# Kernel tuning notes

Hardware: AMD Instinct MI355X
Metric: run time of the kernel (lower is better)

## Reference

```python
import jax, jax.numpy as jnp
import numpy as np

D, K, B, IMG, NCH = 128, 512, 8, 128, 3


def adder2d(x, w, k, stride, pad):
    # AdderNet L1 'convolution': y[b,co,l] = -sum_p |patch[b,p,l] - w[co,p]|
    # x: [B,C,H,W], w: [Cout, C*k*k]
    p = jax.lax.conv_general_dilated_patches(x, (k, k), (stride, stride), [(pad, pad), (pad, pad)])
    Bb, P, Ho, Wo = p.shape
    p = p.reshape(Bb, P, Ho * Wo)  # [B, C*k*k, L]
    def one(wc):  # wc: [P] -> [B, L]; sequential over Cout to bound memory
        return -jnp.sum(jnp.abs(p - wc[None, :, None]), axis=1)
    o = jax.lax.map(one, w)  # [Cout, B, L]
    return jnp.transpose(o, (1, 0, 2)).reshape(Bb, w.shape[0], Ho, Wo)


def bn(x, g, b, eps=1e-5):
    # eval-mode BatchNorm2d with running_mean=0, running_var=1
    s = g * jax.lax.rsqrt(jnp.asarray(1.0 + eps, x.dtype))
    return x * s[None, :, None, None] + b[None, :, None, None]


def conv2d(x, w, b, pad):
    y = jax.lax.conv_general_dilated(x, w, (1, 1), [(pad, pad), (pad, pad)],
                                     dimension_numbers=('NCHW', 'OIHW', 'NCHW'))
    return y + b[None, :, None, None]


def up2x(x):  # nn.Upsample(scale_factor=2, bilinear, align_corners=False)
    Bb, C, H, W = x.shape
    return jax.image.resize(x, (Bb, C, 2 * H, 2 * W), method='bilinear')


def adder_resblock(x, w1, w2, g, b):
    # [ReLU, adder3x3, BN, ReLU, adder1x1] + residual
    h = jax.nn.relu(x)
    h = adder2d(h, w1, 3, 1, 1)
    h = bn(h, g, b)
    h = jax.nn.relu(h)
    h = adder2d(h, w2, 1, 1, 0)
    return x + h


def conv_resblock(x, w1, b1, w2, b2):
    # [ReLU, conv3x3, ReLU, conv1x1] + residual (bn=False in decoder)
    h = jax.nn.relu(x)
    h = conv2d(h, w1, b1, 1)
    h = jax.nn.relu(h)
    h = conv2d(h, w2, b2, 0)
    return x + h


def vq_forward(z_e, E):
    # NearestEmbed: E is [d, k]
    Bb, C, H, W = z_e.shape
    flat = jnp.transpose(z_e, (0, 2, 3, 1)).reshape(-1, C)  # [N, d]
    d2 = (jnp.sum(flat * flat, axis=1, keepdims=True)
          - 2.0 * (flat @ E) + jnp.sum(E * E, axis=0)[None, :])  # [N, k]
    argmin = jnp.argmin(d2, axis=1)  # [N]
    q = jnp.take(E.T, argmin, axis=0)  # [N, d]
    # weight_sg=True path: straight-through to z_e, no grad to E
    zq_flat = flat + jax.lax.stop_gradient(q - flat)
    z_q = jnp.transpose(zq_flat.reshape(Bb, H, W, C), (0, 3, 1, 2))
    # emb path: z_e detached, grad flows to E through the gather
    emb = jnp.transpose(q.reshape(Bb, H, W, C), (0, 3, 1, 2))
    return z_q, emb, argmin.reshape(Bb, H, W)


def reference(x, we1, we2, ae1_w1, ae1_w2, ae2_w1, ae2_w2, bn_gamma, bn_beta,
              emb_weight, rd1_w1, rd1_b1, rd1_w2, rd1_b2, rd2_w1, rd2_b1,
              rd2_w2, rd2_b2, cd1_w, cd1_b, cd2_w, cd2_b):
    g, b = bn_gamma, bn_beta
    h = adder2d(x, we1, 4, 2, 1)
    h = jax.nn.relu(bn(h, g[0], b[0]))
    h = adder2d(h, we2, 4, 2, 1)
    h = jax.nn.relu(bn(h, g[1], b[1]))
    h = adder_resblock(h, ae1_w1, ae1_w2, g[2], b[2])
    h = bn(h, g[3], b[3])
    h = adder_resblock(h, ae2_w1, ae2_w2, g[4], b[4])
    z_e = bn(h, g[5], b[5])  # bne4 (gamma = 1/40)

    z_q, emb, argmin = vq_forward(z_e, emb_weight)

    y = conv_resblock(z_q, rd1_w1, rd1_b1, rd1_w2, rd1_b2)
    y = bn(y, g[6], b[6])
    y = conv_resblock(y, rd2_w1, rd2_b1, rd2_w2, rd2_b2)
    y = up2x(y)
    y = conv2d(y, cd1_w, cd1_b, 1)
    y = jax.nn.relu(bn(y, g[7], b[7]))
    y = up2x(y)
    y = conv2d(y, cd2_w, cd2_b, 1)
    y = jnp.tanh(y)
    return (y, z_e, emb, argmin)


def setup_inputs() -> dict:
    key = jax.random.key(0)
    ks = jax.random.split(key, 16)
    f = lambda k, shp: (0.02 * jax.random.normal(k, shp)).astype(jnp.float32)
    inp = {}
    inp['x'] = jax.random.normal(ks[0], (B, NCH, IMG, IMG), jnp.float32)
    inp['we1'] = f(ks[1], (D, NCH * 16))       # adder 4x4 s2
    inp['we2'] = f(ks[2], (D, D * 16))
    inp['ae1_w1'] = f(ks[3], (D, D * 9))       # adder 3x3
    inp['ae1_w2'] = f(ks[4], (D, D))           # adder 1x1
    inp['ae2_w1'] = f(ks[5], (D, D * 9))
    inp['ae2_w2'] = f(ks[6], (D, D))
    inp['bn_gamma'] = jnp.ones((8, D), jnp.float32).at[5].set(1.0 / 40.0)
    inp['bn_beta'] = jnp.zeros((8, D), jnp.float32)
    inp['emb_weight'] = f(ks[7], (D, K))
    inp['rd1_w1'] = f(ks[8], (D, D, 3, 3)); inp['rd1_b1'] = jnp.zeros(D, jnp.float32)
    inp['rd1_w2'] = f(ks[9], (D, D, 1, 1)); inp['rd1_b2'] = jnp.zeros(D, jnp.float32)
    inp['rd2_w1'] = f(ks[10], (D, D, 3, 3)); inp['rd2_b1'] = jnp.zeros(D, jnp.float32)
    inp['rd2_w2'] = f(ks[11], (D, D, 1, 1)); inp['rd2_b2'] = jnp.zeros(D, jnp.float32)
    inp['cd1_w'] = f(ks[12], (D, D, 3, 3)); inp['cd1_b'] = jnp.zeros(D, jnp.float32)
    inp['cd2_w'] = f(ks[13], (NCH, D, 3, 3)); inp['cd2_b'] = jnp.zeros(NCH, jnp.float32)
    return inp
```

## Files before the change

kernel.cpp:

```cpp
#include <hip/hip_runtime.h>
#include <math.h>

constexpr int Dc = 128;
constexpr int Kc = 512;
constexpr int Bc = 8;

template<int ISADD, int K, int STRIDE, int PAD, int IT, int EPI, int CIN, int CH,
         int OUT_ROWS, int WOUT, int WIN, int HIN, int HOUT>
__global__ __launch_bounds__(256)
void lds_layer(const float* __restrict__ x, const float* __restrict__ w,
               const float* __restrict__ bias,
               const float* __restrict__ itG, const float* __restrict__ itB,
               const float* __restrict__ res,
               const float* __restrict__ rG, const float* __restrict__ rB,
               const float* __restrict__ oG, const float* __restrict__ oB,
               float* __restrict__ out) {
  constexpr int PW = 2;
  constexpr int COBW = 4;
  constexpr int KK = K * K;
  constexpr int SPAN = (PW - 1) * STRIDE + K;
  constexpr int IN_ROWS = (OUT_ROWS - 1) * STRIDE + K;
  constexpr int WPAD = (WOUT - 1) * STRIDE + K;
  constexpr int WLDS = WPAD | 1;
  constexpr int PGW = WOUT / PW;
  static_assert(OUT_ROWS * PGW == 64, "one wave covers the pixel tile");
  constexpr int NCG = Dc / (4 * COBW);
  constexpr int NBAND = HOUT / OUT_ROWS;
  constexpr int NELEM = CH * IN_ROWS * WIN;
  static_assert(NELEM % 256 == 0, "staging divides block");
  constexpr int NIT = NELEM / 256;
  const float r15 = rsqrtf(1.0f + 1e-5f);

  __shared__ float lds[CH][IN_ROWS][WLDS];

  int tid = threadIdx.x;
  int gb = blockIdx.x;
  int cg = gb % NCG;
  int band = (gb / NCG) % NBAND;
  int b = gb / (NCG * NBAND);
  int wv = __builtin_amdgcn_readfirstlane(tid >> 6);
  int lane = tid & 63;
  int co0 = cg * (4 * COBW) + wv * COBW;
  int pr = lane / PGW, pc = lane % PGW;
  int oh = band * OUT_ROWS + pr;
  int ow0 = pc * PW;
  int yi0 = band * OUT_ROWS * STRIDE - PAD;

  for (int e = tid; e < CH * IN_ROWS * WLDS; e += 256) ((float*)lds)[e] = 0.f;

  float acc[PW][COBW];
#pragma unroll
  for (int p = 0; p < PW; ++p)
#pragma unroll
    for (int j = 0; j < COBW; ++j)
      acc[p][j] = ISADD ? 0.f : bias[co0 + j];

  const float* xb = x + (long)b * CIN * HIN * WIN;
  float rbuf[NIT];

  auto stage = [&](int c0) {
#pragma unroll
    for (int it = 0; it < NIT; ++it) {
      int e = it * 256 + tid;
      int col = e % WIN;
      int r = (e / WIN) % IN_ROWS;
      int ch = e / (WIN * IN_ROWS);
      int yi = yi0 + r;
      float v = 0.f;
      if (yi >= 0 && yi < HIN) {
        v = xb[((long)(c0 + ch) * HIN + yi) * WIN + col];
        if (IT == 1) v = fmaxf(v, 0.f);
        if (IT == 2) v = fmaxf(fmaf(v, itG[c0 + ch] * r15, itB[c0 + ch]), 0.f);
      }
      rbuf[it] = v;
    }
  };
  auto towrite = [&]() {
#pragma unroll
    for (int it = 0; it < NIT; ++it) {
      int e = it * 256 + tid;
      int col = e % WIN;
      int r = (e / WIN) % IN_ROWS;
      int ch = e / (WIN * IN_ROWS);
      lds[ch][r][col + PAD] = rbuf[it];
    }
  };

  stage(0);
  for (int c0 = 0; c0 < CIN; c0 += CH) {
    __syncthreads();
    towrite();
    __syncthreads();
    if (c0 + CH < CIN) stage(c0 + CH);
    for (int ch = 0; ch < CH; ++ch) {
      float vbuf[K][SPAN];
#pragma unroll
      for (int kh = 0; kh < K; ++kh)
#pragma unroll
        for (int s = 0; s < SPAN; ++s)
          vbuf[kh][s] = lds[ch][pr * STRIDE + kh][ow0 * STRIDE + s];
      const float* wc = w + ((long)co0 * CIN + (c0 + ch)) * KK;
#pragma unroll
      for (int kh = 0; kh < K; ++kh)
#pragma unroll
        for (int kw = 0; kw < K; ++kw)
#pragma unroll
          for (int j = 0; j < COBW; ++j) {
            float ww = wc[(long)j * CIN * KK + kh * K + kw];
#pragma unroll
            for (int p = 0; p < PW; ++p) {
              float v = vbuf[kh][p * STRIDE + kw];
              if (ISADD) acc[p][j] += fabsf(v - ww);
              else       acc[p][j] = fmaf(v, ww, acc[p][j]);
            }
          }
    }
  }

  long obase = ((long)(b * Dc + co0) * HOUT + oh) * WOUT + ow0;
  float* ob = out + obase;
  const float* rp = (EPI == 2 || EPI == 3 || EPI == 6) ? res + obase : nullptr;
  constexpr long hw = (long)HOUT * WOUT;
#pragma unroll
  for (int j = 0; j < COBW; ++j) {
    float og = 0.f, obb = 0.f, rg = 0.f, rbb = 0.f;
    if (EPI == 1 || EPI == 6) { og = oG[co0 + j] * r15; obb = oB[co0 + j]; }
    if (EPI == 3 || EPI == 6) { rg = rG[co0 + j] * r15; rbb = rB[co0 + j]; }
#pragma unroll
    for (int p = 0; p < PW; ++p) {
      float val = ISADD ? -acc[p][j] : acc[p][j];
      if (EPI == 1) val = fmaxf(fmaf(val, og, obb), 0.f);
      if (EPI == 2) val = rp[j * hw + p] + val;
      if (EPI == 3) val = fmaf(rp[j * hw + p], rg, rbb) + val;
      if (EPI == 5) val = fmaxf(val, 0.f);
      if (EPI == 6) val = fmaf(fmaf(rp[j * hw + p], rg, rbb) + val, og, obb);
      ob[j * hw + p] = val;
    }
  }
}

__device__ __forceinline__ void up_coef(int p, int H, int& i0, int& i1, float& w0, float& w1) {
  int m = p >> 1;
  if ((p & 1) == 0) { i0 = (m > 0) ? m - 1 : 0; i1 = m; w0 = 0.25f; w1 = 0.75f; }
  else              { i0 = m; i1 = (m + 1 < H) ? m + 1 : H - 1; w0 = 0.75f; w1 = 0.25f; }
}

__global__ void up2x_kernel(const float* __restrict__ in, float* __restrict__ out,
                            int C, int H, int W) {
  int H2 = 2 * H, W2 = 2 * W;
  int i = blockIdx.x * blockDim.x + threadIdx.x;
  int total = Bc * C * H2 * W2;
  if (i >= total) return;
  int ow = i % W2; int t = i / W2;
  int oh = t % H2; t /= H2;
  int c = t % C; int b = t / C;
  int y0, y1, x0, x1; float wy0, wy1, wx0, wx1;
  up_coef(oh, H, y0, y1, wy0, wy1);
  up_coef(ow, W, x0, x1, wx0, wx1);
  const float* p = in + (b * C + c) * H * W;
  float v = wy0 * (wx0 * p[y0 * W + x0] + wx1 * p[y0 * W + x1])
          + wy1 * (wx0 * p[y1 * W + x0] + wx1 * p[y1 * W + x1]);
  out[i] = v;
}

__global__ __launch_bounds__(256)
void conv3x3_up_tanh_quad(const float* __restrict__ x, const float* __restrict__ w,
                          const float* __restrict__ bias, float* __restrict__ out,
                          int Hs, int Ws, int Cout) {
  constexpr int CIN = Dc;
  int H2 = 2 * Hs, W2 = 2 * Ws;
  int nq = Hs * Ws;
  int i = blockIdx.x * blockDim.x + threadIdx.x;
  int total = Bc * Cout * nq;
  if (i >= total) return;
  int q = i % nq; int t = i / nq;
  int co = t % Cout; int b = t / Cout;
  int n = q % Ws, m = q / Ws;
  int rows[3] = { (m > 0) ? m - 1 : 0, m, (m + 1 < Hs) ? m + 1 : Hs - 1 };
  int cols[3] = { (n > 0) ? n - 1 : 0, n, (n + 1 < Ws) ? n + 1 : Ws - 1 };
  float rv[4] = { (2 * m - 1 >= 0) ? 1.f : 0.f, 1.f, 1.f, (2 * m + 2 < H2) ? 1.f : 0.f };
  float cv[4] = { (2 * n - 1 >= 0) ? 1.f : 0.f, 1.f, 1.f, (2 * n + 2 < W2) ? 1.f : 0.f };
  float bco = bias[co];
  float acc[4] = { bco, bco, bco, bco };
  const float* xb = x + b * CIN * nq;
  const float* wb = w + co * CIN * 9;
  for (int c = 0; c < CIN; ++c) {
    const float* xc = xb + c * nq;
    float s[3][3];
#pragma unroll
    for (int a = 0; a < 3; ++a)
#pragma unroll
      for (int e = 0; e < 3; ++e) s[a][e] = xc[rows[a] * Ws + cols[e]];
    float rb[4][3];
#pragma unroll
    for (int e = 0; e < 3; ++e) {
      rb[0][e] = fmaf(0.75f, s[0][e], 0.25f * s[1][e]);
      rb[1][e] = fmaf(0.25f, s[0][e], 0.75f * s[1][e]);
      rb[2][e] = fmaf(0.75f, s[1][e], 0.25f * s[2][e]);
      rb[3][e] = fmaf(0.25f, s[1][e], 0.75f * s[2][e]);
    }
    float u[4][4];
#pragma unroll
    for (int di = 0; di < 4; ++di) {
      float rm = rv[di];
      u[di][0] = fmaf(0.75f, rb[di][0], 0.25f * rb[di][1]) * rm * cv[0];
      u[di][1] = fmaf(0.25f, rb[di][0], 0.75f * rb[di][1]) * rm * cv[1];
      u[di][2] = fmaf(0.75f, rb[di][1], 0.25f * rb[di][2]) * rm * cv[2];
      u[di][3] = fmaf(0.25f, rb[di][1], 0.75f * rb[di][2]) * rm * cv[3];
    }
    const float* wc = wb + c * 9;
#pragma unroll
    for (int kh = 0; kh < 3; ++kh)
#pragma unroll
      for (int kw = 0; kw < 3; ++kw) {
        float ww = wc[kh * 3 + kw];
        acc[0] = fmaf(u[kh][kw],         ww, acc[0]);
        acc[1] = fmaf(u[kh][kw + 1],     ww, acc[1]);
        acc[2] = fmaf(u[kh + 1][kw],     ww, acc[2]);
        acc[3] = fmaf(u[kh + 1][kw + 1], ww, acc[3]);
      }
  }
  float* ob = out + (b * Cout + co) * H2 * W2 + (2 * m) * W2 + 2 * n;
  ob[0] = tanhf(acc[0]);      ob[1] = tanhf(acc[1]);
  ob[W2] = tanhf(acc[2]);     ob[W2 + 1] = tanhf(acc[3]);
}

__global__ void vq_e2_kernel(const float* __restrict__ E, float* __restrict__ e2) {
  int k = blockIdx.x * blockDim.x + threadIdx.x;
  if (k >= Kc) return;
  float s = 0.f;
  for (int d = 0; d < Dc; ++d) { float v = E[d * Kc + k]; s += v * v; }
  e2[k] = s;
}

__global__ __launch_bounds__(256)
void vq_kernel8(const float* __restrict__ z_e, const float* __restrict__ E,
                const float* __restrict__ e2,
                float* __restrict__ emb, float* __restrict__ argmin_out) {
  constexpr int HW = 1024;
  __shared__ float f[8][Dc];
  __shared__ float d2s[8][256];
  __shared__ int   ks[8][256];
  int tid = threadIdx.x;
  int n0 = blockIdx.x * 8;
  int b = n0 >> 10;
  int rem = n0 & 1023;
  const float* zb = z_e + (long)b * Dc * HW + rem;
#pragma unroll
  for (int i = 0; i < 4; ++i) {
    int e = i * 256 + tid;
    int p = e & 7, d = e >> 3;
    f[p][d] = zb[d * HW + p];
  }
  __syncthreads();
  float f2 = 0.f;
  if (tid < 8) {
    for (int d = 0; d < Dc; ++d) f2 += f[tid][d] * f[tid][d];
    d2s[tid][0] = f2;
  }
  __syncthreads();
  float f2v[8];
#pragma unroll
  for (int p = 0; p < 8; ++p) f2v[p] = d2s[p][0];
  __syncthreads();

  float best[8]; int bk[8];
#pragma unroll
  for (int p = 0; p < 8; ++p) { best[p] = 3.4e38f; bk[p] = 0; }
  for (int kk = tid; kk < Kc; kk += 256) {
    float dot[8];
#pragma unroll
    for (int p = 0; p < 8; ++p) dot[p] = 0.f;
    for (int d = 0; d < Dc; ++d) {
      float ed = E[d * Kc + kk];
#pragma unroll
      for (int p = 0; p < 8; ++p) dot[p] = fmaf(f[p][d], ed, dot[p]);
    }
    float e2k = e2[kk];
#pragma unroll
    for (int p = 0; p < 8; ++p) {
      float d2 = f2v[p] - 2.f * dot[p] + e2k;
      if (d2 < best[p] || (d2 == best[p] && kk < bk[p])) { best[p] = d2; bk[p] = kk; }
    }
  }
#pragma unroll
  for (int p = 0; p < 8; ++p) { d2s[p][tid] = best[p]; ks[p][tid] = bk[p]; }
  __syncthreads();
  for (int s = 128; s > 0; s >>= 1) {
    if (tid < s) {
#pragma unroll
      for (int p = 0; p < 8; ++p) {
        float ob = d2s[p][tid + s]; int ok = ks[p][tid + s];
        if (ob < d2s[p][tid] || (ob == d2s[p][tid] && ok < ks[p][tid])) {
          d2s[p][tid] = ob; ks[p][tid] = ok;
        }
      }
    }
    __syncthreads();
  }
  if (tid < 8) argmin_out[n0 + tid] = (float)ks[tid][0];
  float* eb = emb + (long)b * Dc * HW + rem;
#pragma unroll
  for (int i = 0; i < 4; ++i) {
    int e = i * 256 + tid;
    int p = e & 7, d = e >> 3;
    eb[d * HW + p] = E[d * Kc + ks[p][0]];
  }
}

extern "C" void kernel_launch(void* const* d_in, const int* in_sizes, int n_in,
                              void* d_out, int out_size, void* d_ws, size_t ws_size,
                              hipStream_t stream) {
  const float* x      = (const float*)d_in[0];
  const float* we1    = (const float*)d_in[1];
  const float* we2    = (const float*)d_in[2];
  const float* ae1_w1 = (const float*)d_in[3];
  const float* ae1_w2 = (const float*)d_in[4];
  const float* ae2_w1 = (const float*)d_in[5];
  const float* ae2_w2 = (const float*)d_in[6];
  const float* bn_g   = (const float*)d_in[7];
  const float* bn_b   = (const float*)d_in[8];
  const float* embw   = (const float*)d_in[9];
  const float* rd1_w1 = (const float*)d_in[10];
  const float* rd1_b1 = (const float*)d_in[11];
  const float* rd1_w2 = (const float*)d_in[12];
  const float* rd1_b2 = (const float*)d_in[13];
  const float* rd2_w1 = (const float*)d_in[14];
  const float* rd2_b1 = (const float*)d_in[15];
  const float* rd2_w2 = (const float*)d_in[16];
  const float* rd2_b2 = (const float*)d_in[17];
  const float* cd1_w  = (const float*)d_in[18];
  const float* cd1_b  = (const float*)d_in[19];
  const float* cd2_w  = (const float*)d_in[20];
  const float* cd2_b  = (const float*)d_in[21];

  const float* g0 = bn_g + 0 * Dc; const float* b0 = bn_b + 0 * Dc;
  const float* g1 = bn_g + 1 * Dc; const float* b1 = bn_b + 1 * Dc;
  const float* g2 = bn_g + 2 * Dc; const float* b2 = bn_b + 2 * Dc;
  const float* g3 = bn_g + 3 * Dc; const float* b3 = bn_b + 3 * Dc;
  const float* g4 = bn_g + 4 * Dc; const float* b4 = bn_b + 4 * Dc;
  const float* g5 = bn_g + 5 * Dc; const float* b5 = bn_b + 5 * Dc;
  const float* g6 = bn_g + 6 * Dc; const float* b6 = bn_b + 6 * Dc;
  const float* g7 = bn_g + 7 * Dc; const float* b7 = bn_b + 7 * Dc;

  float* W64a = (float*)d_ws;
  float* W64b = W64a + 4194304;
  float* Wa   = W64b + 4194304;
  float* Wb   = Wa + 1048576;
  float* Wc   = Wb + 1048576;
  float* e2b  = W64b;

  float* out_y   = (float*)d_out;
  float* out_ze  = out_y  + 393216;
  float* out_emb = out_ze + 1048576;
  float* out_am  = out_emb + 1048576;

  const int TB = 256;
  auto nb = [](int n) { return (n + 255) / 256; };
  const int N64 = Bc * Dc * 64 * 64;
  const float* nul = nullptr;

  const int G32   = Bc * 8 * 8;
  const int G64r2 = Bc * 32 * 8;

  lds_layer<1,4,2,1, 0,1, 3,3, 2,64,128,128,64><<<G64r2, TB, 0, stream>>>(
      x, we1, nul, nul, nul, nul, nul, nul, g0, b0, W64a);
  lds_layer<1,4,2,1, 0,1, Dc,8, 4,32,64,64,32><<<G32, TB, 0, stream>>>(
      W64a, we2, nul, nul, nul, nul, nul, nul, g1, b1, Wa);
  lds_layer<1,3,1,1, 0,1, Dc,16, 4,32,32,32,32><<<G32, TB, 0, stream>>>(
      Wa, ae1_w1, nul, nul, nul, nul, nul, nul, g2, b2, Wb);
  lds_layer<1,1,1,0, 0,2, Dc,32, 4,32,32,32,32><<<G32, TB, 0, stream>>>(
      Wb, ae1_w2, nul, nul, nul, Wa, nul, nul, nul, nul, Wc);
  lds_layer<1,3,1,1, 2,1, Dc,16, 4,32,32,32,32><<<G32, TB, 0, stream>>>(
      Wc, ae2_w1, nul, g3, b3, nul, nul, nul, g4, b4, Wb);
  lds_layer<1,1,1,0, 0,6, Dc,32, 4,32,32,32,32><<<G32, TB, 0, stream>>>(
      Wb, ae2_w2, nul, nul, nul, Wc, g3, b3, g5, b5, out_ze);

  vq_e2_kernel<<<2, 256, 0, stream>>>(embw, e2b);
  vq_kernel8<<<Bc * 1024 / 8, 256, 0, stream>>>(out_ze, embw, e2b, out_emb, out_am);

  lds_layer<0,3,1,1, 1,5, Dc,16, 4,32,32,32,32><<<G32, TB, 0, stream>>>(
      out_emb, rd1_w1, rd1_b1, nul, nul, nul, nul, nul, nul, nul, Wb);
  lds_layer<0,1,1,0, 0,2, Dc,32, 4,32,32,32,32><<<G32, TB, 0, stream>>>(
      Wb, rd1_w2, rd1_b2, nul, nul, out_emb, nul, nul, nul, nul, Wa);
  lds_layer<0,3,1,1, 2,5, Dc,16, 4,32,32,32,32><<<G32, TB, 0, stream>>>(
      Wa, rd2_w1, rd2_b1, g6, b6, nul, nul, nul, nul, nul, Wb);
  lds_layer<0,1,1,0, 0,3, Dc,32, 4,32,32,32,32><<<G32, TB, 0, stream>>>(
      Wb, rd2_w2, rd2_b2, nul, nul, Wa, g6, b6, nul, nul, Wc);

  up2x_kernel<<<nb(N64), TB, 0, stream>>>(Wc, W64a, Dc, 32, 32);
  lds_layer<0,3,1,1, 0,1, Dc,16, 2,64,64,64,64><<<G64r2, TB, 0, stream>>>(
      W64a, cd1_w, cd1_b, nul, nul, nul, nul, nul, g7, b7, W64b);

  conv3x3_up_tanh_quad<<<nb(Bc * 3 * 64 * 64), TB, 0, stream>>>(W64b, cd2_w, cd2_b, out_y, 64, 64, 3);
}
```

Measured before the change: 972.3 us.

## Vectorize LDS staging loads, double channel chunk sizes, reorder block indexing

Global-to-LDS staging now uses float4 loads, with a guard for element counts that do not divide the block, instead of scalar loads. Each layer's channel chunk per stage is doubled, which halves the number of sync/stage rounds but doubles LDS use and staging registers, and that can cut occupancy. The block index mapping now puts channel group outermost, so blocks that share a channel group run next to each other and reuse weights better in cache.

After: 942.9 us. 3.0% less time.

```diff
diff --git a/kernel.cpp b/kernel.cpp
--- a/kernel.cpp
+++ b/kernel.cpp
@@ -26,18 +26,20 @@
   static_assert(OUT_ROWS * PGW == 64, "one wave covers the pixel tile");
   constexpr int NCG = Dc / (4 * COBW);
   constexpr int NBAND = HOUT / OUT_ROWS;
-  constexpr int NELEM = CH * IN_ROWS * WIN;
-  static_assert(NELEM % 256 == 0, "staging divides block");
-  constexpr int NIT = NELEM / 256;
+  constexpr int W4 = WIN / 4;
+  constexpr int NELEM4 = CH * IN_ROWS * W4;
+  constexpr int NIT4 = (NELEM4 + 255) / 256;
+  constexpr bool EXACT = (NELEM4 % 256) == 0;
   const float r15 = rsqrtf(1.0f + 1e-5f);
 
   __shared__ float lds[CH][IN_ROWS][WLDS];
 
   int tid = threadIdx.x;
   int gb = blockIdx.x;
-  int cg = gb % NCG;
-  int band = (gb / NCG) % NBAND;
-  int b = gb / (NCG * NBAND);
+  int cg = gb / (Bc * NBAND);
+  int rem = gb % (Bc * NBAND);
+  int band = rem % NBAND;
+  int b = rem / NBAND;
   int wv = __builtin_amdgcn_readfirstlane(tid >> 6);
   int lane = tid & 63;
   int co0 = cg * (4 * COBW) + wv * COBW;
@@ -56,33 +58,46 @@
       acc[p][j] = ISADD ? 0.f : bias[co0 + j];
 
   const float* xb = x + (long)b * CIN * HIN * WIN;
-  float rbuf[NIT];
+  float4 rbuf[NIT4];
 
   auto stage = [&](int c0) {
 #pragma unroll
-    for (int it = 0; it < NIT; ++it) {
+    for (int it = 0; it < NIT4; ++it) {
       int e = it * 256 + tid;
-      int col = e % WIN;
-      int r = (e / WIN) % IN_ROWS;
-      int ch = e / (WIN * IN_ROWS);
+      if (!EXACT && e >= NELEM4) break;
+      int c4 = e % W4;
+      int r = (e / W4) % IN_ROWS;
+      int ch = e / (W4 * IN_ROWS);
       int yi = yi0 + r;
-      float v = 0.f;
+      float4 v = make_float4(0.f, 0.f, 0.f, 0.f);
       if (yi >= 0 && yi < HIN) {
-        v = xb[((long)(c0 + ch) * HIN + yi) * WIN + col];
-        if (IT == 1) v = fmaxf(v, 0.f);
-        if (IT == 2) v = fmaxf(fmaf(v, itG[c0 + ch] * r15, itB[c0 + ch]), 0.f);
+        v = *(const float4*)&xb[((long)(c0 + ch) * HIN + yi) * WIN + 4 * c4];
+        if (IT == 1) {
+          v.x = fmaxf(v.x, 0.f); v.y = fmaxf(v.y, 0.f);
+          v.z = fmaxf(v.z, 0.f); v.w = fmaxf(v.w, 0.f);
+        }
+        if (IT == 2) {
+          float sc = itG[c0 + ch] * r15, bc = itB[c0 + ch];
+          v.x = fmaxf(fmaf(v.x, sc, bc), 0.f);
+          v.y = fmaxf(fmaf(v.y, sc, bc), 0.f);
+          v.z = fmaxf(fmaf(v.z, sc, bc), 0.f);
+          v.w = fmaxf(fmaf(v.w, sc, bc), 0.f);
+        }
       }
       rbuf[it] = v;
     }
   };
   auto towrite = [&]() {
 #pragma unroll
-    for (int it = 0; it < NIT; ++it) {
+    for (int it = 0; it < NIT4; ++it) {
       int e = it * 256 + tid;
-      int col = e % WIN;
-      int r = (e / WIN) % IN_ROWS;
-      int ch = e / (WIN * IN_ROWS);
-      lds[ch][r][col + PAD] = rbuf[it];
+      if (!EXACT && e >= NELEM4) break;
+      int c4 = e % W4;
+      int r = (e / W4) % IN_ROWS;
+      int ch = e / (W4 * IN_ROWS);
+      float* p = &lds[ch][r][4 * c4 + PAD];
+      float4 v = rbuf[it];
+      p[0] = v.x; p[1] = v.y; p[2] = v.z; p[3] = v.w;
     }
   };
 
@@ -365,27 +380,27 @@
 
   lds_layer<1,4,2,1, 0,1, 3,3, 2,64,128,128,64><<<G64r2, TB, 0, stream>>>(
       x, we1, nul, nul, nul, nul, nul, nul, g0, b0, W64a);
-  lds_layer<1,4,2,1, 0,1, Dc,8, 4,32,64,64,32><<<G32, TB, 0, stream>>>(
+  lds_layer<1,4,2,1, 0,1, Dc,16, 4,32,64,64,32><<<G32, TB, 0, stream>>>(
       W64a, we2, nul, nul, nul, nul, nul, nul, g1, b1, Wa);
-  lds_layer<1,3,1,1, 0,1, Dc,16, 4,32,32,32,32><<<G32, TB, 0, stream>>>(
+  lds_layer<1,3,1,1, 0,1, Dc,32, 4,32,32,32,32><<<G32, TB, 0, stream>>>(
       Wa, ae1_w1, nul, nul, nul, nul, nul, nul, g2, b2, Wb);
-  lds_layer<1,1,1,0, 0,2, Dc,32, 4,32,32,32,32><<<G32, TB, 0, stream>>>(
+  lds_layer<1,1,1,0, 0,2, Dc,64, 4,32,32,32,32><<<G32, TB, 0, stream>>>(
       Wb, ae1_w2, nul, nul, nul, Wa, nul, nul, nul, nul, Wc);
-  lds_layer<1,3,1,1, 2,1, Dc,16, 4,32,32,32,32><<<G32, TB, 0, stream>>>(
+  lds_layer<1,3,1,1, 2,1, Dc,32, 4,32,32,32,32><<<G32, TB, 0, stream>>>(
       Wc, ae2_w1, nul, g3, b3, nul, nul, nul, g4, b4, Wb);
-  lds_layer<1,1,1,0, 0,6, Dc,32, 4,32,32,32,32><<<G32, TB, 0, stream>>>(
+  lds_layer<1,1,1,0, 0,6, Dc,64, 4,32,32,32,32><<<G32, TB, 0, stream>>>(
       Wb, ae2_w2, nul, nul, nul, Wc, g3, b3, g5, b5, out_ze);
 
   vq_e2_kernel<<<2, 256, 0, stream>>>(embw, e2b);
   vq_kernel8<<<Bc * 1024 / 8, 256, 0, stream>>>(out_ze, embw, e2b, out_emb, out_am);
 
-  lds_layer<0,3,1,1, 1,5, Dc,16, 4,32,32,32,32><<<G32, TB, 0, stream>>>(
+  lds_layer<0,3,1,1, 1,5, Dc,32, 4,32,32,32,32><<<G32, TB, 0, stream>>>(
       out_emb, rd1_w1, rd1_b1, nul, nul, nul, nul, nul, nul, nul, Wb);
-  lds_layer<0,1,1,0, 0,2, Dc,32, 4,32,32,32,32><<<G32, TB, 0, stream>>>(
+  lds_layer<0,1,1,0, 0,2, Dc,64, 4,32,32,32,32><<<G32, TB, 0, stream>>>(
       Wb, rd1_w2, rd1_b2, nul, nul, out_emb, nul, nul, nul, nul, Wa);
-  lds_layer<0,3,1,1, 2,5, Dc,16, 4,32,32,32,32><<<G32, TB, 0, stream>>>(
+  lds_layer<0,3,1,1, 2,5, Dc,32, 4,32,32,32,32><<<G32, TB, 0, stream>>>(
       Wa, rd2_w1, rd2_b1, g6, b6, nul, nul, nul, nul, nul, Wb);
-  lds_layer<0,1,1,0, 0,3, Dc,32, 4,32,32,32,32><<<G32, TB, 0, stream>>>(
+  lds_layer<0,1,1,0, 0,3, Dc,64, 4,32,32,32,32><<<G32, TB, 0, stream>>>(
       Wb, rd2_w2, rd2_b2, nul, nul, Wa, g6, b6, nul, nul, Wc);
 
   up2x_kernel<<<nb(N64), TB, 0, stream>>>(Wc, W64a, Dc, 32, 32);
```
